# Performance work log

Measured on AMD Instinct MI355X. Metric: run time of the kernel, lower is better.

Reference implementation:

```python
import jax, jax.numpy as jnp
import numpy as np

MUL = 512
DIMS = (1, 3, 5, 7)  # dims of irreps 0e,1o,2e,3o
N = 8192
TOTAL = MUL * sum(DIMS)  # 8192


def setup_inputs() -> dict:
    key = jax.random.key(0)
    ks = jax.random.split(key, 5)
    inp = {"x": jax.random.normal(ks[0], (N, TOTAL), dtype=jnp.float32)}
    for i in range(4):
        inp[f"w{i}"] = jax.random.normal(ks[i + 1], (MUL, MUL), dtype=jnp.float32)
    return inp


def reference(x, w0, w1, w2, w3):
    # Block-diagonal equivariant linear: for each irrep segment (mul_ir layout),
    # mix multiplicities with a (mul_in, mul_out) weight shared across the
    # (2l+1) irrep components, scaled by 1/sqrt(mul_in).
    ws = (w0, w1, w2, w3)
    scale = 1.0 / np.sqrt(MUL)
    outs = []
    off = 0
    for d, w in zip(DIMS, ws):
        seg = x[:, off:off + MUL * d].reshape(N, MUL, d)  # [N, mul, d]
        o = jnp.einsum('nud,uv->nvd', seg, w,
                       precision=jax.lax.Precision.HIGH) * scale
        outs.append(o.reshape(N, MUL * d))
        off += MUL * d
    return jnp.concatenate(outs, axis=1)  # [N, TOTAL]
```

## Files before the change

### kernel.cpp

```cpp
#include <hip/hip_runtime.h>
#include <hip/hip_bf16.h>
#include <stdint.h>

typedef float  f32x4   __attribute__((ext_vector_type(4)));
typedef short  short8  __attribute__((ext_vector_type(8)));
typedef short  short4v __attribute__((ext_vector_type(4)));

#define TOTAL 8192

__device__ __forceinline__ void dma16(const void* g, void* l) {
  __builtin_amdgcn_global_load_lds(
      (const __attribute__((address_space(1))) unsigned int*)g,
      (__attribute__((address_space(3))) unsigned int*)l,
      16, 0, 0);
}

#define WAITV(N) do { asm volatile("s_waitcnt vmcnt(" #N ")" ::: "memory"); \
                      __builtin_amdgcn_sched_barrier(0); } while (0)
#define WAITL0() asm volatile("s_waitcnt lgkmcnt(0)" ::: "memory")
#define BAR()    __builtin_amdgcn_s_barrier()

__global__ __launch_bounds__(256) void prep_wt(
    const float* __restrict__ w0, const float* __restrict__ w1,
    const float* __restrict__ w2, const float* __restrict__ w3,
    __hip_bfloat16* __restrict__ wt) {
  __shared__ float T[64][65];
  const int s = blockIdx.z;
  const float* w = (s == 0) ? w0 : (s == 1) ? w1 : (s == 2) ? w2 : w3;
  const int u0 = blockIdx.y * 64, v0 = blockIdx.x * 64;
  const int tx = threadIdx.x & 63, ty = threadIdx.x >> 6;
#pragma unroll
  for (int k = 0; k < 16; ++k) {
    int r = ty * 16 + k;
    T[r][tx] = w[(size_t)(u0 + r) * 512 + v0 + tx];
  }
  __syncthreads();
  const float scale = 0.04419417382415922f;
#pragma unroll
  for (int rep = 0; rep < 2; ++rep) {
    int idx = rep * 256 + threadIdx.x;
    int r   = idx >> 3;
    int kc  = idx & 7;
    int ksw = (kc & 4) | ((kc & 3) ^ ((r >> 1) & 3));
    __hip_bfloat16 t8[8];
#pragma unroll
    for (int i = 0; i < 8; ++i) t8[i] = __float2bfloat16(T[kc * 8 + i][r] * scale);
    *(short8*)&wt[((size_t)s << 18) + (size_t)(v0 + r) * 512 + u0 + ksw * 8] =
        *(const short8*)t8;
  }
}

template <int D, int SEGOFF>
__device__ __forceinline__ void seg_gemm(
    const float* __restrict__ x, const __hip_bfloat16* __restrict__ wt,
    float* __restrict__ out, int rt) {
  constexpr int BM = 64, BK = 32, LDA = BK + 8;
  constexpr int CHUNK = BK * D;
  constexpr int ASZ = BM * LDA;
  constexpr int BSZ = 512 * BK;
  constexpr int NPF = (D == 1) ? 2 : 3;
  extern __shared__ char smem[];
  __hip_bfloat16* As0 = (__hip_bfloat16*)smem;
  __hip_bfloat16* As1 = As0 + ASZ;
  __hip_bfloat16* Bs0 = As0 + 2 * ASZ;
  __hip_bfloat16* Bs1 = Bs0 + BSZ;

  const int tid  = threadIdx.x;
  const int lane = tid & 63;
  const int wv   = tid >> 6;
  const int row0 = rt * BM;
  const int nF   = row0 / D;
  const int nL   = (row0 + BM - 1) / D;
  const int F4   = ((nL - nF + 1) * CHUNK) >> 2;
  const int q  = lane >> 4, cl = lane & 15;
  const int slotx = (q ^ ((cl >> 1) & 3)) << 3;

  const float* abase[NPF];
  int aoff[NPF][4];
#pragma unroll
  for (int i = 0; i < NPF; ++i) {
    int e  = tid + (i << 8);
    int ec = e < F4 ? e : 0;
    int p4 = ec << 2;
    int nb = p4 / CHUNK;
    int p  = p4 - nb * CHUNK;
    int n  = nF + nb;
    abase[i] = x + (size_t)n * TOTAL + SEGOFF + p;
    if (D == 1) {
      aoff[i][0] = (e < F4) ? ((n - row0) * LDA + p) : -1;
    } else {
#pragma unroll
      for (int c = 0; c < 4; ++c) {
        int pc = p + c;
        int u  = pc / D;
        int j  = pc - u * D;
        int r  = n * D + j - row0;
        aoff[i][c] = (e < F4 && (unsigned)r < (unsigned)BM) ? (r * LDA + u) : -1;
      }
    }
  }

  f32x4 acc[4][8] = {};

  auto issueA = [&](float4 (&pf)[NPF], int k0) {
#pragma unroll
    for (int i = 0; i < NPF; ++i)
      pf[i] = *(const float4*)(abase[i] + k0 * D);
  };
  auto storeA = [&](__hip_bfloat16* Ab, float4 (&pf)[NPF]) {
#pragma unroll
    for (int i = 0; i < NPF; ++i) {
      if (D == 1) {
        if (aoff[i][0] >= 0) {
          __hip_bfloat16 t4[4];
          t4[0] = __float2bfloat16(pf[i].x); t4[1] = __float2bfloat16(pf[i].y);
          t4[2] = __float2bfloat16(pf[i].z); t4[3] = __float2bfloat16(pf[i].w);
          *(short4v*)&Ab[aoff[i][0]] = *(const short4v*)t4;
        }
      } else {
        const float* vf = (const float*)&pf[i];
#pragma unroll
        for (int c = 0; c < 4; ++c)
          if (aoff[i][c] >= 0) Ab[aoff[i][c]] = __float2bfloat16(vf[c]);
      }
    }
  };
  auto dmaB = [&](__hip_bfloat16* Bb, int k0) {
#pragma unroll
    for (int t8 = 0; t8 < 8; ++t8) {
      int i = wv * 8 + t8;
      int vrow = i * 16 + (lane >> 2);
      dma16(wt + (size_t)vrow * 512 + k0 + ((lane & 3) << 3), Bb + i * 512);
    }
  };
  auto compute = [&](const __hip_bfloat16* Ac, const __hip_bfloat16* Bc) {
    short8 afr[4];
#pragma unroll
    for (int mi = 0; mi < 4; ++mi) {
      const __hip_bfloat16* pa = Ac + (mi * 16 + cl) * LDA + q * 8;
      short4v lo = *(const short4v*)pa;
      short4v hi = *(const short4v*)(pa + 4);
      afr[mi] = __builtin_shufflevector(lo, hi, 0, 1, 2, 3, 4, 5, 6, 7);
    }
#pragma unroll
    for (int ni = 0; ni < 8; ++ni) {
      const short8 bfr = *(const short8*)(Bc + (wv * 128 + ni * 16 + cl) * BK + slotx);
#pragma unroll
      for (int mi = 0; mi < 4; ++mi)
        acc[mi][ni] = __builtin_amdgcn_mfma_f32_16x16x32_bf16(afr[mi], bfr, acc[mi][ni], 0, 0, 0);
    }
  };

  float4 pf_a[NPF], pf_b[NPF];
  issueA(pf_a, 0);
  dmaB(Bs0, 0);
  issueA(pf_b, BK);
  WAITV(11);
  storeA(As0, pf_a);
  WAITL0(); BAR();

  for (int t = 0; t < 16; t += 2) {
    dmaB(Bs1, ((t + 1) & 15) * BK);
    issueA(pf_a, ((t + 2) & 15) * BK);
    WAITV(14);
    compute(As0, Bs0);
    WAITV(11);
    storeA(As1, pf_b);
    WAITL0(); BAR();
    dmaB(Bs0, ((t + 2) & 15) * BK);
    issueA(pf_b, ((t + 3) & 15) * BK);
    WAITV(14);
    compute(As1, Bs1);
    WAITV(11);
    storeA(As0, pf_a);
    WAITL0(); BAR();
  }
  asm volatile("s_waitcnt vmcnt(0)" ::: "memory");

#pragma unroll
  for (int mi = 0; mi < 4; ++mi) {
#pragma unroll
    for (int ni = 0; ni < 8; ++ni) {
#pragma unroll
      for (int rg = 0; rg < 4; ++rg) {
        int R = row0 + mi * 16 + q * 4 + rg;
        int n = R / D;
        int j = R - n * D;
        int v = wv * 128 + ni * 16 + cl;
        out[(size_t)n * TOTAL + SEGOFF + v * D + j] = acc[mi][ni][rg];
      }
    }
  }
}

__global__ __launch_bounds__(256, 2) void linear_main(
    const float* __restrict__ x, const __hip_bfloat16* __restrict__ wt,
    float* __restrict__ out) {
  int bx = blockIdx.x;
  if (bx < 128)        seg_gemm<1, 0>   (x, wt,             out, bx);
  else if (bx < 512)   seg_gemm<3, 512> (x, wt + (1 << 18), out, bx - 128);
  else if (bx < 1152)  seg_gemm<5, 2048>(x, wt + (2 << 18), out, bx - 512);
  else                 seg_gemm<7, 4608>(x, wt + (3 << 18), out, bx - 1152);
}

#define LDS_BYTES 75776

extern "C" void kernel_launch(void* const* d_in, const int* in_sizes, int n_in,
                              void* d_out, int out_size, void* d_ws, size_t ws_size,
                              hipStream_t stream) {
  const float* x  = (const float*)d_in[0];
  const float* w0 = (const float*)d_in[1];
  const float* w1 = (const float*)d_in[2];
  const float* w2 = (const float*)d_in[3];
  const float* w3 = (const float*)d_in[4];
  __hip_bfloat16* wt = (__hip_bfloat16*)d_ws;
  float* out = (float*)d_out;

  hipFuncSetAttribute((const void*)linear_main,
                      hipFuncAttributeMaxDynamicSharedMemorySize, LDS_BYTES);

  hipLaunchKernelGGL(prep_wt, dim3(8, 8, 4), dim3(256), 0, stream,
                     w0, w1, w2, w3, wt);
  hipLaunchKernelGGL(linear_main, dim3(2048), dim3(256), LDS_BYTES, stream,
                     x, wt, out);
}
```

Baseline: 530.2 us.

## Double row tile to 128 with 512 threads and LDS-staged coalesced epilogue

Raises the block tile from 64 to 128 rows and uses 8 waves per block, so each weight tile loaded into LDS is reused across twice as many rows, halving weight traffic per output. The output is now staged through LDS and written as coalesced float4 rows instead of strided scalar stores, and block indices are remapped so that each group of eight consecutive blocks is spread across all four segments. This costs more LDS and registers (a larger accumulator per wave) and adds extra barriers in the epilogue.

```diff
diff --git a/kernel.cpp b/kernel.cpp
--- a/kernel.cpp
+++ b/kernel.cpp
@@ -54,7 +54,7 @@
 __device__ __forceinline__ void seg_gemm(
     const float* __restrict__ x, const __hip_bfloat16* __restrict__ wt,
     float* __restrict__ out, int rt) {
-  constexpr int BM = 64, BK = 32, LDA = BK + 8;
+  constexpr int BM = 128, BK = 32, LDA = BK + 8;
   constexpr int CHUNK = BK * D;
   constexpr int ASZ = BM * LDA;
   constexpr int BSZ = 512 * BK;
@@ -79,7 +79,7 @@
   int aoff[NPF][4];
 #pragma unroll
   for (int i = 0; i < NPF; ++i) {
-    int e  = tid + (i << 8);
+    int e  = tid + (i << 9);
     int ec = e < F4 ? e : 0;
     int p4 = ec << 2;
     int nb = p4 / CHUNK;
@@ -100,7 +100,7 @@
     }
   }
 
-  f32x4 acc[4][8] = {};
+  f32x4 acc[8][4] = {};
 
   auto issueA = [&](float4 (&pf)[NPF], int k0) {
 #pragma unroll
@@ -127,26 +127,26 @@
   };
   auto dmaB = [&](__hip_bfloat16* Bb, int k0) {
 #pragma unroll
-    for (int t8 = 0; t8 < 8; ++t8) {
-      int i = wv * 8 + t8;
+    for (int t4 = 0; t4 < 4; ++t4) {
+      int i = wv * 4 + t4;
       int vrow = i * 16 + (lane >> 2);
       dma16(wt + (size_t)vrow * 512 + k0 + ((lane & 3) << 3), Bb + i * 512);
     }
   };
   auto compute = [&](const __hip_bfloat16* Ac, const __hip_bfloat16* Bc) {
-    short8 afr[4];
-#pragma unroll
-    for (int mi = 0; mi < 4; ++mi) {
+    short8 afr[8];
+#pragma unroll
+    for (int mi = 0; mi < 8; ++mi) {
       const __hip_bfloat16* pa = Ac + (mi * 16 + cl) * LDA + q * 8;
       short4v lo = *(const short4v*)pa;
       short4v hi = *(const short4v*)(pa + 4);
       afr[mi] = __builtin_shufflevector(lo, hi, 0, 1, 2, 3, 4, 5, 6, 7);
     }
 #pragma unroll
-    for (int ni = 0; ni < 8; ++ni) {
-      const short8 bfr = *(const short8*)(Bc + (wv * 128 + ni * 16 + cl) * BK + slotx);
-#pragma unroll
-      for (int mi = 0; mi < 4; ++mi)
+    for (int ni = 0; ni < 4; ++ni) {
+      const short8 bfr = *(const short8*)(Bc + (wv * 64 + ni * 16 + cl) * BK + slotx);
+#pragma unroll
+      for (int mi = 0; mi < 8; ++mi)
         acc[mi][ni] = __builtin_amdgcn_mfma_f32_16x16x32_bf16(afr[mi], bfr, acc[mi][ni], 0, 0, 0);
     }
   };
@@ -155,55 +155,88 @@
   issueA(pf_a, 0);
   dmaB(Bs0, 0);
   issueA(pf_b, BK);
-  WAITV(11);
+  if constexpr (NPF == 3) { WAITV(7); } else { WAITV(6); }
   storeA(As0, pf_a);
   WAITL0(); BAR();
 
   for (int t = 0; t < 16; t += 2) {
     dmaB(Bs1, ((t + 1) & 15) * BK);
     issueA(pf_a, ((t + 2) & 15) * BK);
-    WAITV(14);
+    if constexpr (NPF == 3) { WAITV(10); } else { WAITV(8); }
     compute(As0, Bs0);
-    WAITV(11);
+    if constexpr (NPF == 3) { WAITV(7); } else { WAITV(6); }
     storeA(As1, pf_b);
     WAITL0(); BAR();
     dmaB(Bs0, ((t + 2) & 15) * BK);
     issueA(pf_b, ((t + 3) & 15) * BK);
-    WAITV(14);
+    if constexpr (NPF == 3) { WAITV(10); } else { WAITV(8); }
     compute(As1, Bs1);
-    WAITV(11);
+    if constexpr (NPF == 3) { WAITV(7); } else { WAITV(6); }
     storeA(As0, pf_a);
     WAITL0(); BAR();
   }
   asm volatile("s_waitcnt vmcnt(0)" ::: "memory");
-
-#pragma unroll
-  for (int mi = 0; mi < 4; ++mi) {
-#pragma unroll
-    for (int ni = 0; ni < 8; ++ni) {
-#pragma unroll
-      for (int rg = 0; rg < 4; ++rg) {
-        int R = row0 + mi * 16 + q * 4 + rg;
-        int n = R / D;
-        int j = R - n * D;
-        int v = wv * 128 + ni * 16 + cl;
-        out[(size_t)n * TOTAL + SEGOFF + v * D + j] = acc[mi][ni][rg];
-      }
-    }
-  }
-}
-
-__global__ __launch_bounds__(256, 2) void linear_main(
+  BAR();
+
+  float* Cs = (float*)smem;
+#pragma unroll
+  for (int ch = 0; ch < 4; ++ch) {
+    const int Glo = row0 + ch * 32;
+#pragma unroll
+    for (int mm = 0; mm < 2; ++mm) {
+      const int r0 = mm * 16 + q * 4;
+#pragma unroll
+      for (int ni = 0; ni < 4; ++ni) {
+        const int v = wv * 64 + ni * 16 + cl;
+        *(f32x4*)&Cs[v * 36 + r0] = acc[ch * 2 + mm][ni];
+      }
+    }
+    WAITL0(); BAR();
+    const int n0 = Glo / D, n1 = (Glo + 31) / D;
+    for (int n = n0; n <= n1; ++n) {
+      int jlo = Glo - n * D;       if (jlo < 0) jlo = 0;
+      int jhi = Glo + 32 - n * D;  if (jhi > D) jhi = D;
+      float* orow = out + (size_t)n * TOTAL + SEGOFF;
+      if (jlo == 0 && jhi == D) {
+        const int rb = n * D - Glo;
+        for (int c4 = tid; c4 < 128 * D; c4 += 512) {
+          int c = c4 << 2;
+          float4 f;
+          float* fp = (float*)&f;
+#pragma unroll
+          for (int k = 0; k < 4; ++k) {
+            int cc = c + k;
+            int v = cc / D;
+            int j = cc - v * D;
+            fp[k] = Cs[v * 36 + rb + j];
+          }
+          *(float4*)&orow[c] = f;
+        }
+      } else {
+        const int nj = jhi - jlo;
+        for (int e = tid; e < nj * 512; e += 512) {
+          int j = jlo + (e >> 9);
+          int v = e & 511;
+          orow[v * D + j] = Cs[v * 36 + (n * D + j - Glo)];
+        }
+      }
+    }
+    BAR();
+  }
+}
+
+__global__ __launch_bounds__(512, 2) void linear_main(
     const float* __restrict__ x, const __hip_bfloat16* __restrict__ wt,
     float* __restrict__ out) {
-  int bx = blockIdx.x;
-  if (bx < 128)        seg_gemm<1, 0>   (x, wt,             out, bx);
-  else if (bx < 512)   seg_gemm<3, 512> (x, wt + (1 << 18), out, bx - 128);
-  else if (bx < 1152)  seg_gemm<5, 2048>(x, wt + (2 << 18), out, bx - 512);
-  else                 seg_gemm<7, 4608>(x, wt + (3 << 18), out, bx - 1152);
-}
-
-#define LDS_BYTES 75776
+  int bx  = blockIdx.x;
+  int wid = (bx & 7) * 128 + (bx >> 3);
+  if (wid < 64)        seg_gemm<1, 0>   (x, wt,             out, wid);
+  else if (wid < 256)  seg_gemm<3, 512> (x, wt + (1 << 18), out, wid - 64);
+  else if (wid < 576)  seg_gemm<5, 2048>(x, wt + (2 << 18), out, wid - 256);
+  else                 seg_gemm<7, 4608>(x, wt + (3 << 18), out, wid - 576);
+}
+
+#define LDS_BYTES 86016
 
 extern "C" void kernel_launch(void* const* d_in, const int* in_sizes, int n_in,
                               void* d_out, int out_size, void* d_ws, size_t ws_size,
@@ -221,6 +254,6 @@
 
   hipLaunchKernelGGL(prep_wt, dim3(8, 8, 4), dim3(256), 0, stream,
                      w0, w1, w2, w3, wt);
-  hipLaunchKernelGGL(linear_main, dim3(2048), dim3(256), LDS_BYTES, stream,
+  hipLaunchKernelGGL(linear_main, dim3(1024), dim3(512), LDS_BYTES, stream,
                      x, wt, out);
 }
```

Result: faster. 503.3 us (-5.1%).
